# Kernel tuning notes

Hardware: AMD Instinct MI355X
Metric: run time of the kernel (lower is better)

## Reference

```python
import jax, jax.numpy as jnp
import numpy as np

N_NODES = 100000
N_EDGES = 1600000
IN_DIM, HID, OUT_DIM = 128, 64, 1


def _sage_conv(x, src, dst, wl, wr, b, num_nodes):
    # PyG SAGEConv (aggr='mean', root_weight=True):
    #   out = lin_l(mean_{j in N(i)} x_j) + lin_r(x_i), bias lives in lin_l
    msgs = x[src]                                                  # [E, d] gather
    agg = jax.ops.segment_sum(msgs, dst, num_segments=num_nodes)  # [N, d]
    deg = jax.ops.segment_sum(jnp.ones((src.shape[0],), x.dtype), dst,
                              num_segments=num_nodes)              # [N]
    agg = agg / jnp.maximum(deg, 1.0)[:, None]                     # mean aggregation
    return agg @ wl + x @ wr + b


def setup_inputs() -> dict:
    key = jax.random.key(0)
    ks = jax.random.split(key, 12)
    x = jax.random.normal(ks[0], (N_NODES, IN_DIM), dtype=jnp.float32)
    edge_index = jax.random.randint(ks[1], (2, N_EDGES), 0, N_NODES, dtype=jnp.int64)

    def glorot(k, fan_in, fan_out):
        s = jnp.sqrt(2.0 / (fan_in + fan_out)).astype(jnp.float32)
        return jax.random.normal(k, (fan_in, fan_out), dtype=jnp.float32) * s

    return {
        "x": x,
        "edge_index": edge_index,
        "wl0": glorot(ks[2], IN_DIM, HID), "wr0": glorot(ks[3], IN_DIM, HID),
        "b0": jnp.zeros((HID,), jnp.float32),
        "wl1": glorot(ks[4], HID, HID), "wr1": glorot(ks[5], HID, HID),
        "b1": jnp.zeros((HID,), jnp.float32),
        "wl2": glorot(ks[6], HID, OUT_DIM), "wr2": glorot(ks[7], HID, OUT_DIM),
        "b2": jnp.zeros((OUT_DIM,), jnp.float32),
    }


def reference(x, edge_index, wl0, wr0, b0, wl1, wr1, b1, wl2, wr2, b2):
    src, dst = edge_index[0], edge_index[1]
    n = x.shape[0]
    # layer 0: conv -> relu (dropout is identity in eval mode)
    h = jax.nn.relu(_sage_conv(x, src, dst, wl0, wr0, b0, n))
    # layer 1
    h = jax.nn.relu(_sage_conv(h, src, dst, wl1, wr1, b1, n))
    # final layer + sigmoid
    h = _sage_conv(h, src, dst, wl2, wr2, b2, n)
    return jax.nn.sigmoid(h)
```

## Files before the change

### kernel.cpp

```cpp
#include <hip/hip_runtime.h>
#include <hip/hip_bf16.h>
#include <math.h>


#define SHIFT 7
#define BKT 128
#define CHUNK 4096

typedef __bf16 bf16_t;
typedef bf16_t bf16x8 __attribute__((ext_vector_type(8)));
typedef float f32x4 __attribute__((ext_vector_type(4)));

#define B16LO(u) __uint_as_float((u) << 16)
#define B16HI(u) __uint_as_float((u) & 0xffff0000u)

__global__ __launch_bounds__(256) void hist_bucket(const int* __restrict__ dstv,
                                                   int* __restrict__ bucket_cnt,
                                                   int E, int NB, int nbC,
                                                   const float* __restrict__ wl0,
                                                   const float* __restrict__ wr0,
                                                   const float* __restrict__ wl1,
                                                   const float* __restrict__ wr1,
                                                   bf16_t* __restrict__ w0t,
                                                   bf16_t* __restrict__ w1t) {
    if ((int)blockIdx.x >= nbC) {
        int idx = (blockIdx.x - nbC) * 256 + threadIdx.x;
        if (idx < 128 * 128) {
            int j = idx >> 7, k = idx & 127;
            float v = (j < 64) ? wl0[k * 64 + j] : wr0[k * 64 + (j - 64)];
            w0t[idx] = (bf16_t)v;
        } else if (idx < 128 * 128 + 128 * 64) {
            int i2 = idx - 128 * 128;
            int j = i2 >> 6, k = i2 & 63;
            float v = (j < 64) ? wl1[k * 64 + j] : wr1[k * 64 + (j - 64)];
            w1t[i2] = (bf16_t)v;
        }
        return;
    }
    __shared__ int h[1024];
    for (int i = threadIdx.x; i < NB; i += 256) h[i] = 0;
    __syncthreads();
    int base = blockIdx.x * CHUNK;
#pragma unroll
    for (int k = 0; k < CHUNK / 256; ++k) {
        int e = base + threadIdx.x + k * 256;
        if (e < E) atomicAdd(&h[dstv[e] >> SHIFT], 1);
    }
    __syncthreads();
    for (int i = threadIdx.x; i < NB; i += 256)
        if (h[i]) atomicAdd(&bucket_cnt[i], h[i]);
}

__global__ __launch_bounds__(1024) void scan_bucket(const int* __restrict__ cnt,
                                                    int* __restrict__ boff,
                                                    int* __restrict__ bcur, int NB) {
    __shared__ int s[1024];
    int t = threadIdx.x;
    int v = (t < NB) ? cnt[t] : 0;
    s[t] = v;
    __syncthreads();
    for (int d = 1; d < 1024; d <<= 1) {
        int x = (t >= d) ? s[t - d] : 0;
        __syncthreads();
        s[t] += x;
        __syncthreads();
    }
    if (t < NB) {
        int o = s[t] - v;
        boff[t] = o;
        bcur[t] = o;
    }
    if (t == NB - 1) boff[NB] = s[t];
}

__global__ __launch_bounds__(256) void scatter_bucket(const int* __restrict__ srcv,
                                                      const int* __restrict__ dstv,
                                                      int* __restrict__ bcur,
                                                      int* __restrict__ bucketed,
                                                      int E, int NB) {
    __shared__ int hist[1024];
    __shared__ int offl[1024];
    __shared__ int basel[1024];
    __shared__ int partial[256];
    __shared__ int posA[CHUNK];
    __shared__ int valA[CHUNK];
    const int t = threadIdx.x;
    for (int i = t; i < NB; i += 256) hist[i] = 0;
    __syncthreads();

    const int cbase = blockIdx.x * CHUNK;
    int bk[CHUNK / 256], rk[CHUNK / 256], vv[CHUNK / 256];
#pragma unroll
    for (int k = 0; k < CHUNK / 256; ++k) {
        int e = cbase + t + k * 256;
        if (e < E) {
            int d = dstv[e];
            int s = srcv[e];
            int b = d >> SHIFT;
            bk[k] = b;
            rk[k] = atomicAdd(&hist[b], 1);
            vv[k] = (s << SHIFT) | (d & (BKT - 1));
        } else {
            bk[k] = -1;
        }
    }
    __syncthreads();

    for (int b = t; b < NB; b += 256) {
        int c = hist[b];
        basel[b] = c ? atomicAdd(&bcur[b], c) : 0;
    }
    {
        int g = t * 4;
        int a0 = (g + 0 < NB) ? hist[g + 0] : 0;
        int a1 = (g + 1 < NB) ? hist[g + 1] : 0;
        int a2 = (g + 2 < NB) ? hist[g + 2] : 0;
        int a3 = (g + 3 < NB) ? hist[g + 3] : 0;
        int sum = a0 + a1 + a2 + a3;
        partial[t] = sum;
        __syncthreads();
        for (int d = 1; d < 256; d <<= 1) {
            int x = (t >= d) ? partial[t - d] : 0;
            __syncthreads();
            partial[t] += x;
            __syncthreads();
        }
        int ex = partial[t] - sum;
        if (g + 0 < NB) offl[g + 0] = ex;
        if (g + 1 < NB) offl[g + 1] = ex + a0;
        if (g + 2 < NB) offl[g + 2] = ex + a0 + a1;
        if (g + 3 < NB) offl[g + 3] = ex + a0 + a1 + a2;
    }
    __syncthreads();

    int nloc = E - cbase;
    if (nloc > CHUNK) nloc = CHUNK;
#pragma unroll
    for (int k = 0; k < CHUNK / 256; ++k) {
        if (bk[k] >= 0) {
            int slot = offl[bk[k]] + rk[k];
            posA[slot] = basel[bk[k]] + rk[k];
            valA[slot] = vv[k];
        }
    }
    __syncthreads();
    for (int j = t; j < nloc; j += 256) bucketed[posA[j]] = valA[j];
}

__global__ __launch_bounds__(256) void sort_bucket(const int* __restrict__ bucketed,
                                                   const int* __restrict__ boff,
                                                   int2* __restrict__ od,
                                                   int* __restrict__ csr, int N) {
    __shared__ int cnt[BKT];
    __shared__ int sc[BKT];
    __shared__ int cur[BKT];
    const int b = blockIdx.x;
    const int t = threadIdx.x;
    const int ebase = boff[b], eend = boff[b + 1];
    if (t < BKT) cnt[t] = 0;
    __syncthreads();
    for (int i = ebase + t; i < eend; i += 256)
        atomicAdd(&cnt[bucketed[i] & (BKT - 1)], 1);
    __syncthreads();
    int v = (t < BKT) ? cnt[t] : 0;
    if (t < BKT) sc[t] = v;
    __syncthreads();
    for (int d = 1; d < BKT; d <<= 1) {
        int x = (t < BKT && t >= d) ? sc[t - d] : 0;
        __syncthreads();
        if (t < BKT) sc[t] += x;
        __syncthreads();
    }
    if (t < BKT) {
        int ex = sc[t] - v;
        cur[t] = ex;
        int dst = (b << SHIFT) + t;
        if (dst < N) od[dst] = make_int2(ebase + ex, v);
    }
    __syncthreads();
    for (int i = ebase + t; i < eend; i += 256) {
        int w = bucketed[i];
        int p = atomicAdd(&cur[w & (BKT - 1)], 1);
        csr[ebase + p] = w >> SHIFT;
    }
}

template <int KTOT, bool AIN_BF16>
__global__ __launch_bounds__(256) void gemm_mfma(const void* __restrict__ Ain,
                                                 const bf16_t* __restrict__ Wt,
                                                 bf16_t* __restrict__ Y, int N) {
    const int lane = threadIdx.x & 63;
    const int wv = threadIdx.x >> 6;
    const int r0 = blockIdx.x * 64 + wv * 16;
    const int rr = lane & 15;
    const int quad = lane >> 4;
    const int row_store = r0 + rr;
    int row = (row_store < N) ? row_store : (N - 1);
    constexpr int NK = KTOT / 32;

    bf16x8 xf[NK];
    if (AIN_BF16) {
        const bf16_t* A = (const bf16_t*)Ain;
#pragma unroll
        for (int kk = 0; kk < NK; ++kk)
            xf[kk] = *(const bf16x8*)&A[(size_t)row * KTOT + kk * 32 + quad * 8];
    } else {
        const float* A = (const float*)Ain;
#pragma unroll
        for (int kk = 0; kk < NK; ++kk) {
            const float* ap = &A[(size_t)row * KTOT + kk * 32 + quad * 8];
            float4 f0 = *(const float4*)ap;
            float4 f1 = *(const float4*)(ap + 4);
            union { bf16x8 v; bf16_t h[8]; } u;
            u.h[0] = (bf16_t)f0.x; u.h[1] = (bf16_t)f0.y;
            u.h[2] = (bf16_t)f0.z; u.h[3] = (bf16_t)f0.w;
            u.h[4] = (bf16_t)f1.x; u.h[5] = (bf16_t)f1.y;
            u.h[6] = (bf16_t)f1.z; u.h[7] = (bf16_t)f1.w;
            xf[kk] = u.v;
        }
    }

#pragma unroll
    for (int c = 0; c < 8; ++c) {
        f32x4 acc = {0.f, 0.f, 0.f, 0.f};
#pragma unroll
        for (int kk = 0; kk < NK; ++kk) {
            bf16x8 wf = *(const bf16x8*)&Wt[(size_t)(c * 16 + rr) * KTOT + kk * 32 + quad * 8];
            acc = __builtin_amdgcn_mfma_f32_16x16x32_bf16(wf, xf[kk], acc, 0, 0, 0);
        }
        if (row_store < N) {
            union { bf16_t h[4]; uint2 u; } p;
            p.h[0] = (bf16_t)acc[0]; p.h[1] = (bf16_t)acc[1];
            p.h[2] = (bf16_t)acc[2]; p.h[3] = (bf16_t)acc[3];
            *(uint2*)&Y[(size_t)row_store * 128 + c * 16 + quad * 4] = p.u;
        }
    }
}

template <bool FUSED>
__global__ __launch_bounds__(256) void agg_relu(const bf16_t* __restrict__ y,
                                                const int* __restrict__ csr,
                                                const int2* __restrict__ od,
                                                const float* __restrict__ bias,
                                                bf16_t* __restrict__ h,
                                                const float* __restrict__ wl2,
                                                const float* __restrict__ wr2,
                                                float* __restrict__ sl,
                                                float* __restrict__ sr, int N) {
    const int lane = threadIdx.x & 63;
    const int oct = lane >> 3;
    const int ch = (lane & 7) * 8;
    const int nw = gridDim.x * 4;

    int i = blockIdx.x * 4 + (threadIdx.x >> 6);
    int2 odc = (i < N) ? od[i] : make_int2(0, 0);
    int sidx = 0;
    if (i < N) sidx = (lane < odc.y) ? csr[odc.x + lane] : 0;

    while (i < N) {
        const int inext = i + nw;
        int2 odn = (inext < N) ? od[inext] : make_int2(0, 0);

        const int base = odc.x;
        const int d = odc.y;
        float a0 = 0.f, a1 = 0.f, a2 = 0.f, a3 = 0.f;
        float a4 = 0.f, a5 = 0.f, a6 = 0.f, a7 = 0.f;
        const int nblk = d >> 3;
        const int pm = (nblk < 8) ? nblk : 8;
        int p = 0;
        for (; p + 2 <= pm; p += 2) {
            int s0 = __shfl(sidx, 8 * p + oct);
            int s1 = __shfl(sidx, 8 * p + 8 + oct);
            uint4 v0 = *(const uint4*)&y[(size_t)s0 * 128 + ch];
            uint4 v1 = *(const uint4*)&y[(size_t)s1 * 128 + ch];
            a0 += B16LO(v0.x) + B16LO(v1.x); a1 += B16HI(v0.x) + B16HI(v1.x);
            a2 += B16LO(v0.y) + B16LO(v1.y); a3 += B16HI(v0.y) + B16HI(v1.y);
            a4 += B16LO(v0.z) + B16LO(v1.z); a5 += B16HI(v0.z) + B16HI(v1.z);
            a6 += B16LO(v0.w) + B16LO(v1.w); a7 += B16HI(v0.w) + B16HI(v1.w);
        }
        for (; p < pm; ++p) {
            int s0 = __shfl(sidx, 8 * p + oct);
            uint4 v0 = *(const uint4*)&y[(size_t)s0 * 128 + ch];
            a0 += B16LO(v0.x); a1 += B16HI(v0.x);
            a2 += B16LO(v0.y); a3 += B16HI(v0.y);
            a4 += B16LO(v0.z); a5 += B16HI(v0.z);
            a6 += B16LO(v0.w); a7 += B16HI(v0.w);
        }
        for (; p < nblk; ++p) {
            int s0 = csr[base + 8 * p + oct];
            uint4 v0 = *(const uint4*)&y[(size_t)s0 * 128 + ch];
            a0 += B16LO(v0.x); a1 += B16HI(v0.x);
            a2 += B16LO(v0.y); a3 += B16HI(v0.y);
            a4 += B16LO(v0.z); a5 += B16HI(v0.z);
            a6 += B16LO(v0.w); a7 += B16HI(v0.w);
        }
        {
            int te = 8 * nblk + oct;
            int tec = (te < 64) ? te : 63;
            int s_t = __shfl(sidx, tec);
            if (te < d) {
                int s0 = (te < 64) ? s_t : csr[base + te];
                uint4 v0 = *(const uint4*)&y[(size_t)s0 * 128 + ch];
                a0 += B16LO(v0.x); a1 += B16HI(v0.x);
                a2 += B16LO(v0.y); a3 += B16HI(v0.y);
                a4 += B16LO(v0.z); a5 += B16HI(v0.z);
                a6 += B16LO(v0.w); a7 += B16HI(v0.w);
            }
        }

        int sidxn = 0;
        if (inext < N) sidxn = (lane < odn.y) ? csr[odn.x + lane] : 0;

        a0 += __shfl_xor(a0, 8);  a1 += __shfl_xor(a1, 8);
        a2 += __shfl_xor(a2, 8);  a3 += __shfl_xor(a3, 8);
        a4 += __shfl_xor(a4, 8);  a5 += __shfl_xor(a5, 8);
        a6 += __shfl_xor(a6, 8);  a7 += __shfl_xor(a7, 8);
        a0 += __shfl_xor(a0, 16); a1 += __shfl_xor(a1, 16);
        a2 += __shfl_xor(a2, 16); a3 += __shfl_xor(a3, 16);
        a4 += __shfl_xor(a4, 16); a5 += __shfl_xor(a5, 16);
        a6 += __shfl_xor(a6, 16); a7 += __shfl_xor(a7, 16);
        a0 += __shfl_xor(a0, 32); a1 += __shfl_xor(a1, 32);
        a2 += __shfl_xor(a2, 32); a3 += __shfl_xor(a3, 32);
        a4 += __shfl_xor(a4, 32); a5 += __shfl_xor(a5, 32);
        a6 += __shfl_xor(a6, 32); a7 += __shfl_xor(a7, 32);

        float inv = 1.f / ((d > 0) ? (float)d : 1.f);
        uint4 vs = *(const uint4*)&y[(size_t)i * 128 + 64 + ch];
        float4 bv0 = *(const float4*)&bias[ch];
        float4 bv1 = *(const float4*)&bias[ch + 4];
        float v0 = fmaxf(a0 * inv + B16LO(vs.x) + bv0.x, 0.f);
        float v1 = fmaxf(a1 * inv + B16HI(vs.x) + bv0.y, 0.f);
        float v2 = fmaxf(a2 * inv + B16LO(vs.y) + bv0.z, 0.f);
        float v3 = fmaxf(a3 * inv + B16HI(vs.y) + bv0.w, 0.f);
        float v4 = fmaxf(a4 * inv + B16LO(vs.z) + bv1.x, 0.f);
        float v5 = fmaxf(a5 * inv + B16HI(vs.z) + bv1.y, 0.f);
        float v6 = fmaxf(a6 * inv + B16LO(vs.w) + bv1.z, 0.f);
        float v7 = fmaxf(a7 * inv + B16HI(vs.w) + bv1.w, 0.f);

        if (!FUSED) {
            if (oct == 0) {
                union { bf16_t b[8]; uint4 u; } pk;
                pk.b[0] = (bf16_t)v0; pk.b[1] = (bf16_t)v1;
                pk.b[2] = (bf16_t)v2; pk.b[3] = (bf16_t)v3;
                pk.b[4] = (bf16_t)v4; pk.b[5] = (bf16_t)v5;
                pk.b[6] = (bf16_t)v6; pk.b[7] = (bf16_t)v7;
                *(uint4*)&h[(size_t)i * 64 + ch] = pk.u;
            }
        } else {
            float4 w0 = *(const float4*)&wl2[ch];
            float4 w1 = *(const float4*)&wl2[ch + 4];
            float4 u0 = *(const float4*)&wr2[ch];
            float4 u1 = *(const float4*)&wr2[ch + 4];
            float a = v0 * w0.x + v1 * w0.y + v2 * w0.z + v3 * w0.w +
                      v4 * w1.x + v5 * w1.y + v6 * w1.z + v7 * w1.w;
            float b = v0 * u0.x + v1 * u0.y + v2 * u0.z + v3 * u0.w +
                      v4 * u1.x + v5 * u1.y + v6 * u1.z + v7 * u1.w;
            a += __shfl_xor(a, 1); b += __shfl_xor(b, 1);
            a += __shfl_xor(a, 2); b += __shfl_xor(b, 2);
            a += __shfl_xor(a, 4); b += __shfl_xor(b, 4);
            if (lane == 0) { sl[i] = a; sr[i] = b; }
        }

        odc = odn;
        sidx = sidxn;
        i = inext;
    }
}

__global__ __launch_bounds__(256) void final_k(const float* __restrict__ sl,
                                               const float* __restrict__ sr,
                                               const int* __restrict__ csr,
                                               const int2* __restrict__ od,
                                               const float* __restrict__ b2,
                                               float* __restrict__ out, int N) {
    int wid = blockIdx.x * 4 + (threadIdx.x >> 6);
    if (wid >= N) return;
    const int lane = threadIdx.x & 63;
    const int2 odv = od[wid];
    const int base = odv.x;
    const int d = odv.y;
    float acc = 0.f;
    for (int e = lane; e < d; e += 64) acc += sl[csr[base + e]];
#pragma unroll
    for (int off = 32; off; off >>= 1) acc += __shfl_xor(acc, off);
    if (lane == 0) {
        float m = (d > 0) ? (float)d : 1.f;
        float v = acc / m + sr[wid] + b2[0];
        out[wid] = 1.f / (1.f + expf(-v));
    }
}

extern "C" void kernel_launch(void* const* d_in, const int* in_sizes, int n_in,
                              void* d_out, int out_size, void* d_ws, size_t ws_size,
                              hipStream_t stream) {
    const float* x  = (const float*)d_in[0];
    const int*  ei  = (const int*)d_in[1];
    const float* wl0 = (const float*)d_in[2];
    const float* wr0 = (const float*)d_in[3];
    const float* b0  = (const float*)d_in[4];
    const float* wl1 = (const float*)d_in[5];
    const float* wr1 = (const float*)d_in[6];
    const float* b1  = (const float*)d_in[7];
    const float* wl2 = (const float*)d_in[8];
    const float* wr2 = (const float*)d_in[9];
    const float* b2  = (const float*)d_in[10];
    float* out = (float*)d_out;

    const int E = in_sizes[1] / 2;
    const int N = out_size;
    const int* srcv = ei;
    const int* dstv = ei + E;
    const int NB = (N + BKT - 1) >> SHIFT;

    char* ws = (char*)d_ws;
    size_t o = 0;
    auto take = [&](size_t nbytes) -> void* {
        void* p = ws + o;
        o = (o + nbytes + 255) & ~(size_t)255;
        return p;
    };
    int2* od    = (int2*)take((size_t)N * 8);
    int* bcnt   = (int*)take((size_t)(NB + 2) * 4);
    int* boff   = (int*)take((size_t)(NB + 2) * 4);
    int* bcur   = (int*)take((size_t)(NB + 2) * 4);
    int* csr    = (int*)take((size_t)E * 4);
    bf16_t* w0t = (bf16_t*)take(128 * 128 * 2);
    bf16_t* w1t = (bf16_t*)take(128 * 64 * 2);
    bf16_t* y   = (bf16_t*)take((size_t)N * 128 * 2);
    bf16_t* h   = (bf16_t*)take((size_t)N * 64 * 2);
    float* sl   = (float*)take((size_t)N * 4);
    float* sr   = (float*)take((size_t)N * 4);
    int* bucketed = (int*)y;
    (void)ws_size;

    const int nbC = (E + CHUNK - 1) / CHUNK;
    const int nbP = (128 * 128 + 128 * 64 + 255) / 256;
    const int nbW = (N + 3) / 4;
    const int nbG = (N + 63) / 64;
    const int nbA = 2048;

    hipMemsetAsync(bcnt, 0, (size_t)NB * 4, stream);
    hist_bucket<<<nbC + nbP, 256, 0, stream>>>(dstv, bcnt, E, NB, nbC,
                                               wl0, wr0, wl1, wr1, w0t, w1t);
    scan_bucket<<<1, 1024, 0, stream>>>(bcnt, boff, bcur, NB);
    scatter_bucket<<<nbC, 256, 0, stream>>>(srcv, dstv, bcur, bucketed, E, NB);
    sort_bucket<<<NB, 256, 0, stream>>>(bucketed, boff, od, csr, N);

    gemm_mfma<128, false><<<nbG, 256, 0, stream>>>((const void*)x, w0t, y, N);
    agg_relu<false><<<nbA, 256, 0, stream>>>(y, csr, od, b0, h,
                                             nullptr, nullptr, nullptr, nullptr, N);
    gemm_mfma<64, true><<<nbG, 256, 0, stream>>>((const void*)h, w1t, y, N);
    agg_relu<true><<<nbA, 256, 0, stream>>>(y, csr, od, b1, nullptr,
                                            wl2, wr2, sl, sr, N);
    final_k<<<nbW, 256, 0, stream>>>(sl, sr, csr, od, b2, out, N);
}
```

Before: 313.8 us.

## Drop histogram and scan passes with fixed-capacity buckets; fuse layer-0 GEMM into sort

Edges are now scattered straight into fixed-size per-bucket regions (CAP slots each), using an atomic counter per bucket. This removes the separate histogram kernel, the single-block scan kernel and one extra read of the destination array. The layer-0 MFMA GEMM now runs as extra blocks of the bucket-sort kernel, so it can overlap the sort and saves a launch. In exchange the bucketed and CSR buffers are padded to NB*CAP entries and no longer alias y. Nothing checks for overflow, so a bucket that receives more than CAP edges would corrupt memory.

After: 299.2 us. 4.7% less time.

```diff
diff --git a/kernel.cpp b/kernel.cpp
--- a/kernel.cpp
+++ b/kernel.cpp
@@ -6,6 +6,7 @@
 #define SHIFT 7
 #define BKT 128
 #define CHUNK 4096
+#define CAP 4096
 
 typedef __bf16 bf16_t;
 typedef bf16_t bf16x8 __attribute__((ext_vector_type(8)));
@@ -14,15 +15,17 @@
 #define B16LO(u) __uint_as_float((u) << 16)
 #define B16HI(u) __uint_as_float((u) & 0xffff0000u)
 
-__global__ __launch_bounds__(256) void hist_bucket(const int* __restrict__ dstv,
-                                                   int* __restrict__ bucket_cnt,
-                                                   int E, int NB, int nbC,
-                                                   const float* __restrict__ wl0,
-                                                   const float* __restrict__ wr0,
-                                                   const float* __restrict__ wl1,
-                                                   const float* __restrict__ wr1,
-                                                   bf16_t* __restrict__ w0t,
-                                                   bf16_t* __restrict__ w1t) {
+__global__ __launch_bounds__(256) void scatter_prep(const int* __restrict__ srcv,
+                                                    const int* __restrict__ dstv,
+                                                    int* __restrict__ bcnt,
+                                                    int* __restrict__ bucketed,
+                                                    int E, int NB, int nbC,
+                                                    const float* __restrict__ wl0,
+                                                    const float* __restrict__ wr0,
+                                                    const float* __restrict__ wl1,
+                                                    const float* __restrict__ wr1,
+                                                    bf16_t* __restrict__ w0t,
+                                                    bf16_t* __restrict__ w1t) {
     if ((int)blockIdx.x >= nbC) {
         int idx = (blockIdx.x - nbC) * 256 + threadIdx.x;
         if (idx < 128 * 128) {
@@ -37,47 +40,6 @@
         }
         return;
     }
-    __shared__ int h[1024];
-    for (int i = threadIdx.x; i < NB; i += 256) h[i] = 0;
-    __syncthreads();
-    int base = blockIdx.x * CHUNK;
-#pragma unroll
-    for (int k = 0; k < CHUNK / 256; ++k) {
-        int e = base + threadIdx.x + k * 256;
-        if (e < E) atomicAdd(&h[dstv[e] >> SHIFT], 1);
-    }
-    __syncthreads();
-    for (int i = threadIdx.x; i < NB; i += 256)
-        if (h[i]) atomicAdd(&bucket_cnt[i], h[i]);
-}
-
-__global__ __launch_bounds__(1024) void scan_bucket(const int* __restrict__ cnt,
-                                                    int* __restrict__ boff,
-                                                    int* __restrict__ bcur, int NB) {
-    __shared__ int s[1024];
-    int t = threadIdx.x;
-    int v = (t < NB) ? cnt[t] : 0;
-    s[t] = v;
-    __syncthreads();
-    for (int d = 1; d < 1024; d <<= 1) {
-        int x = (t >= d) ? s[t - d] : 0;
-        __syncthreads();
-        s[t] += x;
-        __syncthreads();
-    }
-    if (t < NB) {
-        int o = s[t] - v;
-        boff[t] = o;
-        bcur[t] = o;
-    }
-    if (t == NB - 1) boff[NB] = s[t];
-}
-
-__global__ __launch_bounds__(256) void scatter_bucket(const int* __restrict__ srcv,
-                                                      const int* __restrict__ dstv,
-                                                      int* __restrict__ bcur,
-                                                      int* __restrict__ bucketed,
-                                                      int E, int NB) {
     __shared__ int hist[1024];
     __shared__ int offl[1024];
     __shared__ int basel[1024];
@@ -108,7 +70,7 @@
 
     for (int b = t; b < NB; b += 256) {
         int c = hist[b];
-        basel[b] = c ? atomicAdd(&bcur[b], c) : 0;
+        basel[b] = c ? (b * CAP + atomicAdd(&bcnt[b], c)) : 0;
     }
     {
         int g = t * 4;
@@ -147,68 +109,32 @@
     for (int j = t; j < nloc; j += 256) bucketed[posA[j]] = valA[j];
 }
 
-__global__ __launch_bounds__(256) void sort_bucket(const int* __restrict__ bucketed,
-                                                   const int* __restrict__ boff,
-                                                   int2* __restrict__ od,
-                                                   int* __restrict__ csr, int N) {
+__global__ __launch_bounds__(256) void sort_gemm0(const int* __restrict__ bucketed,
+                                                  const int* __restrict__ bcnt,
+                                                  int2* __restrict__ od,
+                                                  int* __restrict__ csr, int N, int NB,
+                                                  const float* __restrict__ x,
+                                                  const bf16_t* __restrict__ w0t,
+                                                  bf16_t* __restrict__ y) {
     __shared__ int cnt[BKT];
     __shared__ int sc[BKT];
     __shared__ int cur[BKT];
-    const int b = blockIdx.x;
     const int t = threadIdx.x;
-    const int ebase = boff[b], eend = boff[b + 1];
-    if (t < BKT) cnt[t] = 0;
-    __syncthreads();
-    for (int i = ebase + t; i < eend; i += 256)
-        atomicAdd(&cnt[bucketed[i] & (BKT - 1)], 1);
-    __syncthreads();
-    int v = (t < BKT) ? cnt[t] : 0;
-    if (t < BKT) sc[t] = v;
-    __syncthreads();
-    for (int d = 1; d < BKT; d <<= 1) {
-        int x = (t < BKT && t >= d) ? sc[t - d] : 0;
-        __syncthreads();
-        if (t < BKT) sc[t] += x;
-        __syncthreads();
-    }
-    if (t < BKT) {
-        int ex = sc[t] - v;
-        cur[t] = ex;
-        int dst = (b << SHIFT) + t;
-        if (dst < N) od[dst] = make_int2(ebase + ex, v);
-    }
-    __syncthreads();
-    for (int i = ebase + t; i < eend; i += 256) {
-        int w = bucketed[i];
-        int p = atomicAdd(&cur[w & (BKT - 1)], 1);
-        csr[ebase + p] = w >> SHIFT;
-    }
-}
-
-template <int KTOT, bool AIN_BF16>
-__global__ __launch_bounds__(256) void gemm_mfma(const void* __restrict__ Ain,
-                                                 const bf16_t* __restrict__ Wt,
-                                                 bf16_t* __restrict__ Y, int N) {
-    const int lane = threadIdx.x & 63;
-    const int wv = threadIdx.x >> 6;
-    const int r0 = blockIdx.x * 64 + wv * 16;
-    const int rr = lane & 15;
-    const int quad = lane >> 4;
-    const int row_store = r0 + rr;
-    int row = (row_store < N) ? row_store : (N - 1);
-    constexpr int NK = KTOT / 32;
-
-    bf16x8 xf[NK];
-    if (AIN_BF16) {
-        const bf16_t* A = (const bf16_t*)Ain;
-#pragma unroll
-        for (int kk = 0; kk < NK; ++kk)
-            xf[kk] = *(const bf16x8*)&A[(size_t)row * KTOT + kk * 32 + quad * 8];
-    } else {
-        const float* A = (const float*)Ain;
-#pragma unroll
-        for (int kk = 0; kk < NK; ++kk) {
-            const float* ap = &A[(size_t)row * KTOT + kk * 32 + quad * 8];
+
+    if ((int)blockIdx.x >= NB) {
+        const int bid = blockIdx.x - NB;
+        const int lane = t & 63;
+        const int wv = t >> 6;
+        const int r0 = bid * 64 + wv * 16;
+        const int rr = lane & 15;
+        const int quad = lane >> 4;
+        const int row_store = r0 + rr;
+        int row = (row_store < N) ? row_store : (N - 1);
+
+        bf16x8 xf[4];
+#pragma unroll
+        for (int kk = 0; kk < 4; ++kk) {
+            const float* ap = &x[(size_t)row * 128 + kk * 32 + quad * 8];
             float4 f0 = *(const float4*)ap;
             float4 f1 = *(const float4*)(ap + 4);
             union { bf16x8 v; bf16_t h[8]; } u;
@@ -218,14 +144,77 @@
             u.h[6] = (bf16_t)f1.z; u.h[7] = (bf16_t)f1.w;
             xf[kk] = u.v;
         }
-    }
+#pragma unroll
+        for (int c = 0; c < 8; ++c) {
+            f32x4 acc = {0.f, 0.f, 0.f, 0.f};
+#pragma unroll
+            for (int kk = 0; kk < 4; ++kk) {
+                bf16x8 wf = *(const bf16x8*)&w0t[(size_t)(c * 16 + rr) * 128 + kk * 32 + quad * 8];
+                acc = __builtin_amdgcn_mfma_f32_16x16x32_bf16(wf, xf[kk], acc, 0, 0, 0);
+            }
+            if (row_store < N) {
+                union { bf16_t h[4]; uint2 u; } p;
+                p.h[0] = (bf16_t)acc[0]; p.h[1] = (bf16_t)acc[1];
+                p.h[2] = (bf16_t)acc[2]; p.h[3] = (bf16_t)acc[3];
+                *(uint2*)&y[(size_t)row_store * 128 + c * 16 + quad * 4] = p.u;
+            }
+        }
+        return;
+    }
+
+    const int b = blockIdx.x;
+    const int ebase = b * CAP;
+    const int eend = ebase + bcnt[b];
+    if (t < BKT) cnt[t] = 0;
+    __syncthreads();
+    for (int i = ebase + t; i < eend; i += 256)
+        atomicAdd(&cnt[bucketed[i] & (BKT - 1)], 1);
+    __syncthreads();
+    int v = (t < BKT) ? cnt[t] : 0;
+    if (t < BKT) sc[t] = v;
+    __syncthreads();
+    for (int d = 1; d < BKT; d <<= 1) {
+        int xsc = (t < BKT && t >= d) ? sc[t - d] : 0;
+        __syncthreads();
+        if (t < BKT) sc[t] += xsc;
+        __syncthreads();
+    }
+    if (t < BKT) {
+        int ex = sc[t] - v;
+        cur[t] = ex;
+        int dst = (b << SHIFT) + t;
+        if (dst < N) od[dst] = make_int2(ebase + ex, v);
+    }
+    __syncthreads();
+    for (int i = ebase + t; i < eend; i += 256) {
+        int w = bucketed[i];
+        int p = atomicAdd(&cur[w & (BKT - 1)], 1);
+        csr[ebase + p] = w >> SHIFT;
+    }
+}
+
+__global__ __launch_bounds__(256) void gemm1(const bf16_t* __restrict__ A,
+                                             const bf16_t* __restrict__ Wt,
+                                             bf16_t* __restrict__ Y, int N) {
+    const int lane = threadIdx.x & 63;
+    const int wv = threadIdx.x >> 6;
+    const int r0 = blockIdx.x * 64 + wv * 16;
+    const int rr = lane & 15;
+    const int quad = lane >> 4;
+    const int row_store = r0 + rr;
+    int row = (row_store < N) ? row_store : (N - 1);
+
+    bf16x8 xf[2];
+#pragma unroll
+    for (int kk = 0; kk < 2; ++kk)
+        xf[kk] = *(const bf16x8*)&A[(size_t)row * 64 + kk * 32 + quad * 8];
 
 #pragma unroll
     for (int c = 0; c < 8; ++c) {
         f32x4 acc = {0.f, 0.f, 0.f, 0.f};
 #pragma unroll
-        for (int kk = 0; kk < NK; ++kk) {
-            bf16x8 wf = *(const bf16x8*)&Wt[(size_t)(c * 16 + rr) * KTOT + kk * 32 + quad * 8];
+        for (int kk = 0; kk < 2; ++kk) {
+            bf16x8 wf = *(const bf16x8*)&Wt[(size_t)(c * 16 + rr) * 64 + kk * 32 + quad * 8];
             acc = __builtin_amdgcn_mfma_f32_16x16x32_bf16(wf, xf[kk], acc, 0, 0, 0);
         }
         if (row_store < N) {
@@ -419,18 +408,16 @@
         o = (o + nbytes + 255) & ~(size_t)255;
         return p;
     };
-    int2* od    = (int2*)take((size_t)N * 8);
-    int* bcnt   = (int*)take((size_t)(NB + 2) * 4);
-    int* boff   = (int*)take((size_t)(NB + 2) * 4);
-    int* bcur   = (int*)take((size_t)(NB + 2) * 4);
-    int* csr    = (int*)take((size_t)E * 4);
-    bf16_t* w0t = (bf16_t*)take(128 * 128 * 2);
-    bf16_t* w1t = (bf16_t*)take(128 * 64 * 2);
-    bf16_t* y   = (bf16_t*)take((size_t)N * 128 * 2);
-    bf16_t* h   = (bf16_t*)take((size_t)N * 64 * 2);
-    float* sl   = (float*)take((size_t)N * 4);
-    float* sr   = (float*)take((size_t)N * 4);
-    int* bucketed = (int*)y;
+    int2* od      = (int2*)take((size_t)N * 8);
+    int* bcnt     = (int*)take((size_t)(NB + 2) * 4);
+    int* bucketed = (int*)take((size_t)NB * CAP * 4);
+    int* csr      = (int*)take((size_t)NB * CAP * 4);
+    bf16_t* w0t   = (bf16_t*)take(128 * 128 * 2);
+    bf16_t* w1t   = (bf16_t*)take(128 * 64 * 2);
+    bf16_t* y     = (bf16_t*)take((size_t)N * 128 * 2);
+    bf16_t* h     = (bf16_t*)take((size_t)N * 64 * 2);
+    float* sl     = (float*)take((size_t)N * 4);
+    float* sr     = (float*)take((size_t)N * 4);
     (void)ws_size;
 
     const int nbC = (E + CHUNK - 1) / CHUNK;
@@ -440,16 +427,14 @@
     const int nbA = 2048;
 
     hipMemsetAsync(bcnt, 0, (size_t)NB * 4, stream);
-    hist_bucket<<<nbC + nbP, 256, 0, stream>>>(dstv, bcnt, E, NB, nbC,
-                                               wl0, wr0, wl1, wr1, w0t, w1t);
-    scan_bucket<<<1, 1024, 0, stream>>>(bcnt, boff, bcur, NB);
-    scatter_bucket<<<nbC, 256, 0, stream>>>(srcv, dstv, bcur, bucketed, E, NB);
-    sort_bucket<<<NB, 256, 0, stream>>>(bucketed, boff, od, csr, N);
-
-    gemm_mfma<128, false><<<nbG, 256, 0, stream>>>((const void*)x, w0t, y, N);
+    scatter_prep<<<nbC + nbP, 256, 0, stream>>>(srcv, dstv, bcnt, bucketed, E, NB, nbC,
+                                                wl0, wr0, wl1, wr1, w0t, w1t);
+    sort_gemm0<<<NB + nbG, 256, 0, stream>>>(bucketed, bcnt, od, csr, N, NB,
+                                             x, w0t, y);
+
     agg_relu<false><<<nbA, 256, 0, stream>>>(y, csr, od, b0, h,
                                              nullptr, nullptr, nullptr, nullptr, N);
-    gemm_mfma<64, true><<<nbG, 256, 0, stream>>>((const void*)h, w1t, y, N);
+    gemm1<<<nbG, 256, 0, stream>>>(h, w1t, y, N);
     agg_relu<true><<<nbA, 256, 0, stream>>>(y, csr, od, b1, nullptr,
                                             wl2, wr2, sl, sr, N);
     final_k<<<nbW, 256, 0, stream>>>(sl, sr, csr, od, b2, out, N);
```
